# Performance work log

Hardware: AMD Instinct MI355X
Metric: run time of the kernel (lower is better)

The kernel has to match this reference:

```python
import jax, jax.numpy as jnp
import numpy as np

N = 200000   # nodes (Elliptic-scale)
E = 500000   # directed edges
F = 166      # in_channels / node feature dim
H = 128      # hidden_channels
C = 2        # out_channels
T = 49       # number of time steps


def setup_inputs() -> dict:
    key = jax.random.key(0)
    ks = jax.random.split(key, 12)
    x = jax.random.normal(ks[0], (N, F), jnp.float32)
    edge_index = jax.random.randint(ks[1], (2, E), 0, N, dtype=jnp.int32)
    time_step = jax.random.randint(ks[2], (N,), 0, T, dtype=jnp.int32)
    sF = 1.0 / np.sqrt(F)
    sH = 1.0 / np.sqrt(H)
    initial_w = jax.random.uniform(ks[3], (F, F), jnp.float32, -sF, sF)
    gru_w_ih = jax.random.uniform(ks[4], (3 * F, F), jnp.float32, -sF, sF)
    gru_w_hh = jax.random.uniform(ks[5], (3 * F, F), jnp.float32, -sF, sF)
    gru_b_ih = jax.random.uniform(ks[6], (3 * F,), jnp.float32, -sF, sF)
    gru_b_hh = jax.random.uniform(ks[7], (3 * F,), jnp.float32, -sF, sF)
    proj_w = jax.random.uniform(ks[8], (H, F), jnp.float32, -sF, sF)
    proj_b = jax.random.uniform(ks[9], (H,), jnp.float32, -sF, sF)
    cls_w = jax.random.uniform(ks[10], (C, H), jnp.float32, -sH, sH)
    cls_b = jax.random.uniform(ks[11], (C,), jnp.float32, -sH, sH)
    return {"x": x, "edge_index": edge_index, "time_step": time_step,
            "initial_w": initial_w, "gru_w_ih": gru_w_ih, "gru_w_hh": gru_w_hh,
            "gru_b_ih": gru_b_ih, "gru_b_hh": gru_b_hh,
            "proj_w": proj_w, "proj_b": proj_b, "cls_w": cls_w, "cls_b": cls_b}


def reference(x, edge_index, time_step, initial_w, gru_w_ih, gru_w_hh,
              gru_b_ih, gru_b_hh, proj_w, proj_b, cls_w, cls_b):
    src, dst = edge_index[0], edge_index[1]
    n = x.shape[0]

    def gru(W):
        # torch.nn.GRU single step, input = hidden = W  (FxF matrix, rows = batch)
        gi = W @ gru_w_ih.T + gru_b_ih
        gh = W @ gru_w_hh.T + gru_b_hh
        i_r, i_z, i_n = jnp.split(gi, 3, axis=-1)
        h_r, h_z, h_n = jnp.split(gh, 3, axis=-1)
        r = jax.nn.sigmoid(i_r + h_r)
        z = jax.nn.sigmoid(i_z + h_z)
        nn_ = jnp.tanh(i_n + r * h_n)
        return (1.0 - z) * nn_ + z * W

    def step(carry, t):
        W, logits = carry
        W = gru(W)  # evolve GCN weight (EvolveGCN-O)
        # subgraph of nodes with time_step <= t, expressed by masking (same math
        # as relabel+extract: inactive nodes contribute nothing, their outputs are ignored)
        act = time_step <= t
        ew = (act[src] & act[dst]).astype(x.dtype)
        # gcn_norm with self-loops: deg = in-degree over active edges + 1
        deg = jax.ops.segment_sum(ew, dst, num_segments=n) + 1.0
        dinv = jax.lax.rsqrt(deg)
        norm = ew * dinv[src] * dinv[dst]
        h = jnp.where(act[:, None], x, 0.0) @ W               # [N, F]
        agg = jax.ops.segment_sum(h[src] * norm[:, None], dst, num_segments=n)
        agg = agg + h / deg[:, None]                          # self-loop term dinv_i^2 * h_i
        z = jax.nn.relu(agg @ proj_w.T + proj_b)              # [N, H] (dropout: eval mode)
        lg = z @ cls_w.T + cls_b                              # [N, C]
        logits = jnp.where((time_step == t)[:, None], lg, logits)
        return (W, logits), None

    init = (initial_w, jnp.zeros((n, cls_w.shape[0]), x.dtype))
    (_, logits), _ = jax.lax.scan(step, init, jnp.arange(T, dtype=time_step.dtype))
    return logits
```

## Files before the change

kernel.cpp:

```cpp
#include <hip/hip_runtime.h>
#include <hip/hip_fp16.h>
#include <math.h>

#define NN 200000
#define NE 500000
#define FF 166
#define HH 128
#define CC 2
#define TT 49
#define GG 498
#define PADN 203136
#define MAXTILES 6400
#define KP 84
#define KPAD 192
#define SCB 512
#define SNB 391
#define HB 782
#define CIB 1954
#define XSB 37500
#define ECB 782
#define P2B 210
#define C2B 977
#define H2B 391
#define DEGB 782
#define MBB (TT * 96)

typedef _Float16 half2v __attribute__((ext_vector_type(2)));
typedef _Float16 f16x4 __attribute__((ext_vector_type(4)));
typedef _Float16 f16x8 __attribute__((ext_vector_type(8)));
typedef float f32x4 __attribute__((ext_vector_type(4)));
typedef unsigned long long u64;

static __device__ __forceinline__ float fdot2f(half2v a, half2v b, float c) {
#if __has_builtin(__builtin_amdgcn_fdot2)
    return __builtin_amdgcn_fdot2(a, b, c, false);
#else
    return c + (float)a.x * (float)b.x + (float)a.y * (float)b.y;
#endif
}

__global__ __launch_bounds__(512) void setup1(
        const float* __restrict__ wih, const float* __restrict__ whh,
        const float* __restrict__ projw,
        _Float16* __restrict__ wkp, float* __restrict__ projwT,
        const int* __restrict__ dstp, int* __restrict__ offc,
        const int* __restrict__ ts, int* __restrict__ cnt, int* __restrict__ rank) {
    __shared__ int h2[2][TT];
    int b = blockIdx.x;
    int tid = threadIdx.x;
    if (b < P2B) {
        int idx = b * 512 + tid;
        const int A = 2 * KP * 512;
        if (idx < A) {
            int m = idx / (KP * 512);
            int r = idx - m * (KP * 512);
            int kp = r >> 9, c = r & 511;
            const float* Wm = m ? whh : wih;
            float x0 = 0.0f, x1 = 0.0f;
            if (c < GG) {
                int k0 = 2 * kp, k1 = 2 * kp + 1;
                if (k0 < FF) x0 = Wm[c * FF + k0];
                if (k1 < FF) x1 = Wm[c * FF + k1];
            }
            wkp[2 * idx]     = (_Float16)x0;
            wkp[2 * idx + 1] = (_Float16)x1;
        } else if (idx < A + FF * HH) {
            int q = idx - A;
            int k = q >> 7, hh = q & 127;
            projwT[q] = projw[hh * FF + k];
        }
    } else if (b < P2B + C2B) {
        int e = (b - P2B) * 512 + tid;
        if (e < NE) atomicAdd(&offc[dstp[e]], 1);
    } else {
        int hb2 = b - P2B - C2B;
        int sub = tid >> 8;
        int lt = tid & 255;
        if (lt < TT) h2[sub][lt] = 0;
        __syncthreads();
        int i = hb2 * 512 + tid;
        if (i < NN) {
            int t = ts[i];
            rank[i] = atomicAdd(&h2[sub][t], 1);
        }
        __syncthreads();
        if (lt < TT) cnt[(hb2 * 2 + sub) * TT + lt] = h2[sub][lt];
    }
}

__global__ __launch_bounds__(512) void setup2g(
        const float* __restrict__ initial_w, const _Float16* __restrict__ wkp,
        const float* __restrict__ bih, const float* __restrict__ bhh,
        float* __restrict__ W_all,
        const int* __restrict__ off, int* __restrict__ bsum,
        const int* __restrict__ cnt, int* __restrict__ basecol, int* __restrict__ bcnt) {
    __shared__ float s_w[FF];
    __shared__ __align__(16) _Float16 s_wh[2 * KP];
    __shared__ float s_pre[2][512];
    __shared__ int s[512];
    int tid = threadIdx.x;
    int b = blockIdx.x;

    if (b < FF) {
        int row = b;
        if (tid < FF) {
            float v = initial_w[(size_t)row * FF + tid];
            s_w[tid] = v;
            s_wh[tid] = (_Float16)v;
        } else if (tid < 2 * KP) {
            s_wh[tid] = (_Float16)0.0f;
        }
        int cc0 = tid * 2;
        bool act = cc0 < 996;
        int m = (cc0 >= 498) ? 1 : 0;
        int c0 = act ? (cc0 - m * 498) : 0;
        half2v wr0[KP], wr1[KP];
        {
            const half2v* __restrict__ pW =
                (const half2v*)wkp + (size_t)(act ? m : 0) * (KP * 512) + c0;
            #pragma unroll
            for (int kp = 0; kp < KP; ++kp) {
                wr0[kp] = pW[(size_t)(kp << 9)];
                wr1[kp] = pW[(size_t)(kp << 9) + 1];
            }
        }
        float bi_r = 0, bi_z = 0, bi_n = 0, bh_r = 0, bh_z = 0, bh_n = 0;
        if (tid < FF) {
            bi_r = bih[tid]; bi_z = bih[FF + tid]; bi_n = bih[2 * FF + tid];
            bh_r = bhh[tid]; bh_z = bhh[FF + tid]; bh_n = bhh[2 * FF + tid];
        }
        __syncthreads();
        const f16x8* s_wh8 = (const f16x8*)s_wh;
        for (int t = 0; t < TT; ++t) {
            if (act) {
                float a0 = 0.0f, a1 = 0.0f;
                #pragma unroll
                for (int q = 0; q < 21; ++q) {
                    f16x8 w8 = s_wh8[q];
                    half2v h0 = __builtin_shufflevector(w8, w8, 0, 1);
                    half2v h1 = __builtin_shufflevector(w8, w8, 2, 3);
                    half2v h2v = __builtin_shufflevector(w8, w8, 4, 5);
                    half2v h3 = __builtin_shufflevector(w8, w8, 6, 7);
                    a0 = fdot2f(wr0[4 * q + 0], h0, a0);  a1 = fdot2f(wr1[4 * q + 0], h0, a1);
                    a0 = fdot2f(wr0[4 * q + 1], h1, a0);  a1 = fdot2f(wr1[4 * q + 1], h1, a1);
                    a0 = fdot2f(wr0[4 * q + 2], h2v, a0); a1 = fdot2f(wr1[4 * q + 2], h2v, a1);
                    a0 = fdot2f(wr0[4 * q + 3], h3, a0);  a1 = fdot2f(wr1[4 * q + 3], h3, a1);
                }
                s_pre[m][c0]     = a0;
                s_pre[m][c0 + 1] = a1;
            }
            __syncthreads();
            if (tid < FF) {
                float i_r = s_pre[0][tid]          + bi_r;
                float h_r = s_pre[1][tid]          + bh_r;
                float i_z = s_pre[0][FF + tid]     + bi_z;
                float h_z = s_pre[1][FF + tid]     + bh_z;
                float i_n = s_pre[0][2 * FF + tid] + bi_n;
                float h_n = s_pre[1][2 * FF + tid] + bh_n;
                float rg = 1.0f / (1.0f + expf(-(i_r + h_r)));
                float zg = 1.0f / (1.0f + expf(-(i_z + h_z)));
                float ng = tanhf(i_n + rg * h_n);
                float wnew = (1.0f - zg) * ng + zg * s_w[tid];
                s_w[tid] = wnew;
                s_wh[tid] = (_Float16)wnew;
                W_all[((size_t)t * FF + row) * FF + tid] = wnew;
            }
            __syncthreads();
        }
    } else if (b < FF + SNB) {
        int bb = b - FF;
        int i = bb * SCB + tid;
        s[tid] = (i < NN) ? off[i] : 0;
        __syncthreads();
        for (int d = 256; d > 0; d >>= 1) {
            if (tid < d) s[tid] += s[tid + d];
            __syncthreads();
        }
        if (tid == 0) bsum[bb] = s[0];
    } else {
        int t = b - FF - SNB;
        int b0 = tid * 2;
        int v0 = (b0 < HB) ? cnt[b0 * TT + t] : 0;
        int v1 = (b0 + 1 < HB) ? cnt[(b0 + 1) * TT + t] : 0;
        int sum = v0 + v1;
        s[tid] = sum;
        __syncthreads();
        for (int d = 1; d < 512; d <<= 1) {
            int u = (tid >= d) ? s[tid - d] : 0;
            __syncthreads();
            s[tid] += u;
            __syncthreads();
        }
        int base = s[tid] - sum;
        if (b0 < HB) basecol[b0 * TT + t] = base;
        if (b0 + 1 < HB) basecol[(b0 + 1) * TT + t] = base + v0;
        if (tid == 511) bcnt[t] = s[511];
    }
}

__global__ __launch_bounds__(512) void setup3(
        const int* __restrict__ bsum, int* __restrict__ bpre, int* __restrict__ off,
        const int* __restrict__ bcnt, int* __restrict__ pstart,
        int* __restrict__ tile_t, int* __restrict__ tile_r0, int* __restrict__ meta) {
    __shared__ int s[512];
    int tid = threadIdx.x;
    if (blockIdx.x == 0) {
        int v = (tid < SNB) ? bsum[tid] : 0;
        s[tid] = v;
        __syncthreads();
        for (int d = 1; d < 512; d <<= 1) {
            int u = (tid >= d) ? s[tid - d] : 0;
            __syncthreads();
            s[tid] += u;
            __syncthreads();
        }
        bpre[tid] = s[tid] - v;
        if (tid == 511) off[NN] = s[511];
    } else {
        int t = tid;
        int nt = (t < TT) ? (bcnt[t] + 31) / 32 : 0;
        if (t < 64) s[t] = nt;
        __syncthreads();
        for (int d = 1; d < 64; d <<= 1) {
            int v = (t >= d && t < 64) ? s[t - d] : 0;
            __syncthreads();
            if (t < 64) s[t] += v;
            __syncthreads();
        }
        if (t < 64) {
            int ntbase = s[t] - nt;
            int pbase = ntbase * 32;
            if (t < TT) {
                pstart[t] = pbase;
                for (int u = 0; u < nt; ++u) {
                    tile_t[ntbase + u] = t;
                    tile_r0[ntbase + u] = pbase + u * 32;
                }
            }
            if (t == 63) {
                meta[0] = s[63];
                meta[1] = s[63] * 32;
                pstart[TT] = s[63] * 32;
            }
        }
    }
}

__global__ __launch_bounds__(512) void setup4(
        int* __restrict__ off, const int* __restrict__ bpre,
        const int* __restrict__ ts, const int* __restrict__ rank,
        const int* __restrict__ basecol, const int* __restrict__ pstart,
        int* __restrict__ perm, int* __restrict__ pos) {
    __shared__ int s[512];
    int b = blockIdx.x, tid = threadIdx.x;
    if (b < SNB) {
        int i = b * SCB + tid;
        int v = (i < NN) ? off[i] : 0;
        s[tid] = v;
        __syncthreads();
        for (int d = 1; d < 512; d <<= 1) {
            int u = (tid >= d) ? s[tid - d] : 0;
            __syncthreads();
            s[tid] += u;
            __syncthreads();
        }
        if (i < NN) off[i] = s[tid] - v + bpre[b];
    } else {
        int i = (b - SNB) * 512 + tid;
        if (i < NN) {
            int t = ts[i];
            int hb = i >> 8;
            int p = pstart[t] + basecol[hb * TT + t] + rank[i];
            perm[p] = i;
            pos[i] = p;
        }
    }
}

__global__ __launch_bounds__(256) void fill_adj(
        const int* __restrict__ srcp, const int* __restrict__ dstp,
        const int* __restrict__ ts, const int* __restrict__ off,
        int* __restrict__ cursor, int2* __restrict__ adjst,
        const int* __restrict__ pos) {
    int e = blockIdx.x * 256 + threadIdx.x;
    if (e < NE) {
        int d = dstp[e];
        int s2 = srcp[e];
        int p = atomicAdd(&cursor[d], 1);
        adjst[off[d] + p] = make_int2(s2, (ts[s2] << 25) | pos[s2]);
    }
}

__global__ __launch_bounds__(256) void degf_m(
        const int* __restrict__ off, const int2* __restrict__ adjst,
        const int* __restrict__ ts, _Float16* __restrict__ dinvh,
        float* __restrict__ selfdeg,
        const float* __restrict__ W_all, const float* __restrict__ projwT,
        _Float16* __restrict__ Mh) {
    __shared__ unsigned short sh[TT * 256];
    __shared__ __align__(16) float sw2[2][168];
    int b = blockIdx.x;
    int tid = threadIdx.x;
    if (b < DEGB) {
        int i = b * 256 + tid;
        for (int t = 0; t < TT; ++t) sh[t * 256 + tid] = 0;
        if (i >= NN) return;
        int tsi = ts[i];
        int e0 = off[i], e1 = off[i + 1];
        for (int e = e0; e < e1; ++e) {
            int tj = adjst[e].y >> 25;
            sh[tj * 256 + tid]++;
        }
        int cum = 1;
        for (int t = 0; t < TT; ++t) {
            cum += sh[t * 256 + tid];
            dinvh[(size_t)t * NN + i] = (_Float16)rsqrtf((float)cum);
            if (t == tsi) selfdeg[i] = 1.0f / (float)cum;
        }
    } else {
        int mb = b - DEGB;
        int t = mb / 96, rb = mb - t * 96;
        int r0 = rb * 2;
        for (int idx = tid; idx < 2 * FF; idx += 256) {
            int rr = idx / FF, k = idx - rr * FF;
            int r = r0 + rr;
            sw2[rr][k] = (r < FF) ? W_all[((size_t)t * FF + r) * FF + k] : 0.0f;
        }
        __syncthreads();
        int rr = tid >> 7, h = tid & 127;
        int r = r0 + rr;
        float acc = 0.0f;
        if (r < FF) {
            const float* __restrict__ pw = projwT + h;
            #pragma unroll 4
            for (int c4 = 0; c4 < 164; c4 += 4) {
                float4 w = *(const float4*)&sw2[rr][c4];
                acc += w.x * pw[(size_t)(c4 + 0) << 7];
                acc += w.y * pw[(size_t)(c4 + 1) << 7];
                acc += w.z * pw[(size_t)(c4 + 2) << 7];
                acc += w.w * pw[(size_t)(c4 + 3) << 7];
            }
            acc += sw2[rr][164] * pw[(size_t)164 << 7];
            acc += sw2[rr][165] * pw[(size_t)165 << 7];
        }
        Mh[((size_t)t * HH + h) * KPAD + r] = (_Float16)acc;
    }
}

__global__ __launch_bounds__(256) void setup6(
        const int* __restrict__ off, const int2* __restrict__ adjst,
        const int* __restrict__ ts, const _Float16* __restrict__ dinvh,
        int2* __restrict__ ewp, int* __restrict__ nact,
        const float* __restrict__ x, const int* __restrict__ pos,
        f16x4* __restrict__ x2p4) {
    int b = blockIdx.x, tid = threadIdx.x;
    if (b < ECB) {
        int i = b * 256 + tid;
        if (i >= NN) return;
        int t = ts[i];
        const _Float16* dv = dinvh + (size_t)t * NN;
        float dvi = (float)dv[i];
        int e0 = off[i], e1 = off[i + 1];
        int c = e0;
        for (int e = e0; e < e1; ++e) {
            int2 a = adjst[e];
            if ((a.y >> 25) <= t) {
                float w = (float)dv[a.x] * dvi;
                ewp[c++] = make_int2(a.y & 0x1FFFFFF, __float_as_int(w));
            }
        }
        nact[i] = c - e0;
    } else {
        int idx = (b - ECB) * 256 + tid;
        if (idx >= NN * 48) return;
        int i = idx / 48, cp4 = idx - i * 48;
        int c0 = cp4 * 4;
        const float* xr = x + (size_t)i * FF;
        union { u64 u; float f[2]; } p0, p1;
        p0.u = 0; p1.u = 0;
        if (c0 + 3 < FF) {
            p0.u = __builtin_nontemporal_load((const u64*)(xr + c0));
            p1.u = __builtin_nontemporal_load((const u64*)(xr + c0 + 2));
        } else if (c0 < FF) {
            p0.u = __builtin_nontemporal_load((const u64*)(xr + c0));
        }
        f16x4 h;
        h[0] = (_Float16)p0.f[0]; h[1] = (_Float16)p0.f[1];
        h[2] = (_Float16)p1.f[0]; h[3] = (_Float16)p1.f[1];
        x2p4[(size_t)pos[i] * 48 + cp4] = h;
    }
}

__global__ __launch_bounds__(512) void gemm_fused5(
        const int* __restrict__ meta, const int* __restrict__ tile_t,
        const int* __restrict__ tile_r0, const int* __restrict__ perm,
        const float* __restrict__ selfdeg, const f16x4* __restrict__ x2p4,
        const int* __restrict__ off, const int* __restrict__ nact,
        const int2* __restrict__ ewp,
        const _Float16* __restrict__ Mh, const float* __restrict__ proj_b,
        const float* __restrict__ cls_w, const float* __restrict__ cls_b,
        float* __restrict__ out) {
    __shared__ __align__(16) char smraw[32 * 130 * 4];
    _Float16* sY = (_Float16*)smraw;
    float* sP = (float*)smraw;
    int bid = blockIdx.x;
    if (bid >= meta[0]) return;
    int t = tile_t[bid], r0 = tile_r0[bid];
    int tid = threadIdx.x;
    int lane = tid & 63;
    int w = tid >> 6;
    bool ln48 = lane < 48;

    {
        const uint4* src = (const uint4*)(x2p4 + (size_t)r0 * 48);
        #pragma unroll
        for (int u = 0; u < 2; ++u) {
            int q = tid + u * 512;
            if (q < 768) {
                int row = q / 24, kc = q - row * 24;
                *(uint4*)(sY + row * 200 + kc * 8) = src[q];
            }
        }
    }
    __syncthreads();

    int rbase = w * 4;
    int ep[4], ee[4];
    float ac[4][4];
    #pragma unroll
    for (int q = 0; q < 4; ++q) {
        int r = rbase + q;
        int i = perm[r0 + r];
        float sw = 0.0f;
        ep[q] = 0; ee[q] = 0;
        if (i >= 0) {
            sw = selfdeg[i];
            ep[q] = off[i];
            ee[q] = ep[q] + nact[i];
        }
        f16x4 h = (f16x4)((_Float16)0.0f);
        if (ln48) h = *(const f16x4*)(sY + r * 200 + lane * 4);
        ac[q][0] = sw * (float)h[0];
        ac[q][1] = sw * (float)h[1];
        ac[q][2] = sw * (float)h[2];
        ac[q][3] = sw * (float)h[3];
    }
    int2 pc[4];
    #pragma unroll
    for (int q = 0; q < 4; ++q) pc[q] = (ep[q] < ee[q]) ? ewp[ep[q]] : make_int2(0, 0);
    while ((ep[0] < ee[0]) | (ep[1] < ee[1]) | (ep[2] < ee[2]) | (ep[3] < ee[3])) {
        int js[4]; float wv[4];
        #pragma unroll
        for (int q = 0; q < 4; ++q) {
            bool val = ep[q] < ee[q];
            js[q] = pc[q].x;
            wv[q] = val ? __int_as_float(pc[q].y) : 0.0f;
            if (val) ep[q]++;
        }
        #pragma unroll
        for (int q = 0; q < 4; ++q) pc[q] = (ep[q] < ee[q]) ? ewp[ep[q]] : make_int2(0, 0);
        #pragma unroll
        for (int q = 0; q < 4; ++q) {
            if (wv[q] != 0.0f && ln48) {
                f16x4 g = x2p4[(size_t)js[q] * 48 + lane];
                ac[q][0] += wv[q] * (float)g[0];
                ac[q][1] += wv[q] * (float)g[1];
                ac[q][2] += wv[q] * (float)g[2];
                ac[q][3] += wv[q] * (float)g[3];
            }
        }
    }
    #pragma unroll
    for (int q = 0; q < 4; ++q) {
        if (ln48) {
            f16x4 o;
            o[0] = (_Float16)ac[q][0];
            o[1] = (_Float16)ac[q][1];
            o[2] = (_Float16)ac[q][2];
            o[3] = (_Float16)ac[q][3];
            *(f16x4*)(sY + (rbase + q) * 200 + lane * 4) = o;
        }
    }
    __syncthreads();

    int lr = lane & 15;
    int kg = lane >> 4;
    int c0 = w * 16;
    f32x4 acc0 = {0, 0, 0, 0}, acc1 = {0, 0, 0, 0};
    const _Float16* B0 = Mh + ((size_t)t * HH + c0 + lr) * KPAD + kg * 8;
    const _Float16* A0 = sY + lr * 200 + kg * 8;
    const _Float16* A1 = A0 + 16 * 200;

    #pragma unroll
    for (int s = 0; s < 6; ++s) {
        f16x8 b0 = *(const f16x8*)(B0 + s * 32);
        f16x8 a0 = *(const f16x8*)(A0 + s * 32);
        f16x8 a1 = *(const f16x8*)(A1 + s * 32);
        acc0 = __builtin_amdgcn_mfma_f32_16x16x32_f16(a0, b0, acc0, 0, 0, 0);
        acc1 = __builtin_amdgcn_mfma_f32_16x16x32_f16(a1, b0, acc1, 0, 0, 0);
    }

    float pb = proj_b[c0 + lr];
    __syncthreads();
    int prow = kg * 4;
    int colw = c0 + lr;
    #pragma unroll
    for (int r = 0; r < 4; ++r) {
        sP[(prow + r) * 130 + colw]      = fmaxf(acc0[r] + pb, 0.0f);
        sP[(16 + prow + r) * 130 + colw] = fmaxf(acc1[r] + pb, 0.0f);
    }
    __syncthreads();

    int row = tid >> 4, cc = (tid >> 3) & 1, qq = tid & 7;
    const float* pr = sP + row * 130 + qq * 16;
    const float* cw = cls_w + cc * HH + qq * 16;
    float s = 0.0f;
    #pragma unroll
    for (int h = 0; h < 16; ++h) s += pr[h] * cw[h];
    s += __shfl_xor(s, 1);
    s += __shfl_xor(s, 2);
    s += __shfl_xor(s, 4);
    if (qq == 0) {
        int node = perm[r0 + row];
        if (node >= 0) out[(size_t)node * CC + cc] = s + cls_b[cc];
    }
}

extern "C" void kernel_launch(void* const* d_in, const int* in_sizes, int n_in,
                              void* d_out, int out_size, void* d_ws, size_t ws_size,
                              hipStream_t stream) {
    const float* x = (const float*)d_in[0];
    const int* ei = (const int*)d_in[1];
    const int* srcp = ei;
    const int* dstp = ei + NE;
    const int* ts = (const int*)d_in[2];
    const float* initial_w = (const float*)d_in[3];
    const float* wih = (const float*)d_in[4];
    const float* whh = (const float*)d_in[5];
    const float* bih = (const float*)d_in[6];
    const float* bhh = (const float*)d_in[7];
    const float* projw = (const float*)d_in[8];
    const float* projb = (const float*)d_in[9];
    const float* clsw = (const float*)d_in[10];
    const float* clsb = (const float*)d_in[11];
    float* out = (float*)d_out;

    char* base = (char*)d_ws;
    size_t o = 0;
    auto alloc = [&](size_t bytes) { size_t r = o; o = (o + bytes + 255) & ~(size_t)255; return r; };

    float*    W_all   = (float*)   (base + alloc((size_t)TT * FF * FF * 4));
    _Float16* Mh      = (_Float16*)(base + alloc((size_t)TT * HH * KPAD * 2));
    _Float16* wkp     = (_Float16*)(base + alloc((size_t)2 * KP * 512 * 2 * 2));
    float*    projwT  = (float*)   (base + alloc((size_t)FF * HH * 4));
    int*      off     = (int*)     (base + alloc((size_t)(NN + 1) * 4));
    int*      cursor  = (int*)     (base + alloc((size_t)NN * 4));
    int2*     adjst   = (int2*)    (base + alloc((size_t)NE * 8));
    int2*     ewp     = (int2*)    (base + alloc((size_t)NE * 8));
    _Float16* dinvh   = (_Float16*)(base + alloc((size_t)TT * NN * 2));
    float*    selfdeg = (float*)   (base + alloc((size_t)NN * 4));
    int*      nact    = (int*)     (base + alloc((size_t)NN * 4));
    int*      pos     = (int*)     (base + alloc((size_t)NN * 4));
    int*      bcnt    = (int*)     (base + alloc((size_t)TT * 4));
    int*      pstart  = (int*)     (base + alloc((size_t)(TT + 1) * 4));
    int*      meta    = (int*)     (base + alloc(2 * 4));
    int*      tile_t  = (int*)     (base + alloc((size_t)MAXTILES * 4));
    int*      tile_r0 = (int*)     (base + alloc((size_t)MAXTILES * 4));
    int*      perm    = (int*)     (base + alloc((size_t)PADN * 4));
    int*      bsum    = (int*)     (base + alloc((size_t)512 * 4));
    int*      bpre    = (int*)     (base + alloc((size_t)520 * 4));
    int*      cnt     = (int*)     (base + alloc((size_t)HB * TT * 4));
    int*      basecol = (int*)     (base + alloc((size_t)HB * TT * 4));
    int*      rank    = (int*)     (base + alloc((size_t)NN * 4));
    f16x4*    x2p4    = (f16x4*)   (base + alloc((size_t)PADN * 48 * 8));

    hipMemsetAsync(off, 0, (size_t)((char*)cursor - (char*)off) + (size_t)NN * 4, stream);
    hipMemsetAsync(perm, 0xFF, (size_t)PADN * 4, stream);

    setup1<<<P2B + C2B + H2B, 512, 0, stream>>>(wih, whh, projw, wkp, projwT,
                                                dstp, off, ts, cnt, rank);
    setup2g<<<FF + SNB + TT, 512, 0, stream>>>(initial_w, wkp, bih, bhh, W_all,
                                               off, bsum, cnt, basecol, bcnt);
    setup3<<<2, 512, 0, stream>>>(bsum, bpre, off, bcnt, pstart, tile_t, tile_r0, meta);
    setup4<<<SNB + SNB, 512, 0, stream>>>(off, bpre, ts, rank, basecol, pstart, perm, pos);
    fill_adj<<<CIB, 256, 0, stream>>>(srcp, dstp, ts, off, cursor, adjst, pos);
    degf_m<<<DEGB + MBB, 256, 0, stream>>>(off, adjst, ts, dinvh, selfdeg, W_all, projwT, Mh);
    setup6<<<ECB + XSB, 256, 0, stream>>>(off, adjst, ts, dinvh, ewp, nact, x, pos, x2p4);

    gemm_fused5<<<MAXTILES, 512, 0, stream>>>(meta, tile_t, tile_r0, perm, selfdeg,
                                              x2p4, off, nact, ewp, Mh, projb, clsw, clsb, out);
}
```

Before: 318.4 us.

## Build per-time degree counts directly and pack only active edges without CSR

Replaces the full CSR adjacency build (fill_adj, then per-node scans in degf_m and setup6) with atomics into a dense [T,N] degree-count array and an active-degree count per destination. Edge weights are then written straight into an active-only CSR. The Mh projection work moves into setup3 with 4 rows per block, so the pipeline drops two kernel launches and the intermediate adjst array. In exchange it memsets and scans a 39 MB degcnt buffer, and more global atomics run in setup1.

```diff
diff --git a/kernel.cpp b/kernel.cpp
--- a/kernel.cpp
+++ b/kernel.cpp
@@ -18,12 +18,10 @@
 #define HB 782
 #define CIB 1954
 #define XSB 37500
-#define ECB 782
 #define P2B 210
 #define C2B 977
 #define H2B 391
-#define DEGB 782
-#define MBB (TT * 96)
+#define MB3 (TT * 48)
 
 typedef _Float16 half2v __attribute__((ext_vector_type(2)));
 typedef _Float16 f16x4 __attribute__((ext_vector_type(4)));
@@ -43,8 +41,10 @@
         const float* __restrict__ wih, const float* __restrict__ whh,
         const float* __restrict__ projw,
         _Float16* __restrict__ wkp, float* __restrict__ projwT,
-        const int* __restrict__ dstp, int* __restrict__ offc,
-        const int* __restrict__ ts, int* __restrict__ cnt, int* __restrict__ rank) {
+        const int* __restrict__ srcp, const int* __restrict__ dstp,
+        const int* __restrict__ ts,
+        int* __restrict__ degcnt, int* __restrict__ actdeg,
+        int* __restrict__ cnt, int* __restrict__ rank) {
     __shared__ int h2[2][TT];
     int b = blockIdx.x;
     int tid = threadIdx.x;
@@ -71,7 +71,13 @@
         }
     } else if (b < P2B + C2B) {
         int e = (b - P2B) * 512 + tid;
-        if (e < NE) atomicAdd(&offc[dstp[e]], 1);
+        if (e < NE) {
+            int d = dstp[e];
+            int s2 = srcp[e];
+            int tsrc = ts[s2];
+            atomicAdd(&degcnt[(size_t)tsrc * NN + d], 1);
+            if (tsrc <= ts[d]) atomicAdd(&actdeg[d], 1);
+        }
     } else {
         int hb2 = b - P2B - C2B;
         int sub = tid >> 8;
@@ -92,8 +98,10 @@
         const float* __restrict__ initial_w, const _Float16* __restrict__ wkp,
         const float* __restrict__ bih, const float* __restrict__ bhh,
         float* __restrict__ W_all,
-        const int* __restrict__ off, int* __restrict__ bsum,
-        const int* __restrict__ cnt, int* __restrict__ basecol, int* __restrict__ bcnt) {
+        const int* __restrict__ actdeg, int* __restrict__ bsum,
+        const int* __restrict__ cnt, int* __restrict__ basecol, int* __restrict__ bcnt,
+        const int* __restrict__ degcnt, const int* __restrict__ ts,
+        _Float16* __restrict__ dinvh, float* __restrict__ selfdeg) {
     __shared__ float s_w[FF];
     __shared__ __align__(16) _Float16 s_wh[2 * KP];
     __shared__ float s_pre[2][512];
@@ -170,14 +178,14 @@
     } else if (b < FF + SNB) {
         int bb = b - FF;
         int i = bb * SCB + tid;
-        s[tid] = (i < NN) ? off[i] : 0;
+        s[tid] = (i < NN) ? actdeg[i] : 0;
         __syncthreads();
         for (int d = 256; d > 0; d >>= 1) {
             if (tid < d) s[tid] += s[tid + d];
             __syncthreads();
         }
         if (tid == 0) bsum[bb] = s[0];
-    } else {
+    } else if (b < FF + SNB + TT) {
         int t = b - FF - SNB;
         int b0 = tid * 2;
         int v0 = (b0 < HB) ? cnt[b0 * TT + t] : 0;
@@ -195,16 +203,31 @@
         if (b0 < HB) basecol[b0 * TT + t] = base;
         if (b0 + 1 < HB) basecol[(b0 + 1) * TT + t] = base + v0;
         if (tid == 511) bcnt[t] = s[511];
+    } else {
+        int i = (b - FF - SNB - TT) * 512 + tid;
+        if (i < NN) {
+            int tsi = ts[i];
+            int cum = 1;
+            for (int t = 0; t < TT; ++t) {
+                cum += degcnt[(size_t)t * NN + i];
+                dinvh[(size_t)t * NN + i] = (_Float16)rsqrtf((float)cum);
+                if (t == tsi) selfdeg[i] = 1.0f / (float)cum;
+            }
+        }
     }
 }
 
 __global__ __launch_bounds__(512) void setup3(
-        const int* __restrict__ bsum, int* __restrict__ bpre, int* __restrict__ off,
+        const int* __restrict__ bsum, int* __restrict__ bpre,
         const int* __restrict__ bcnt, int* __restrict__ pstart,
-        int* __restrict__ tile_t, int* __restrict__ tile_r0, int* __restrict__ meta) {
+        int* __restrict__ tile_t, int* __restrict__ tile_r0, int* __restrict__ meta,
+        const float* __restrict__ W_all, const float* __restrict__ projwT,
+        _Float16* __restrict__ Mh) {
     __shared__ int s[512];
+    __shared__ __align__(16) float sw4[4][168];
     int tid = threadIdx.x;
-    if (blockIdx.x == 0) {
+    int b = blockIdx.x;
+    if (b == 0) {
         int v = (tid < SNB) ? bsum[tid] : 0;
         s[tid] = v;
         __syncthreads();
@@ -215,8 +238,7 @@
             __syncthreads();
         }
         bpre[tid] = s[tid] - v;
-        if (tid == 511) off[NN] = s[511];
-    } else {
+    } else if (b == 1) {
         int t = tid;
         int nt = (t < TT) ? (bcnt[t] + 31) / 32 : 0;
         if (t < 64) s[t] = nt;
@@ -243,11 +265,39 @@
                 pstart[TT] = s[63] * 32;
             }
         }
+    } else {
+        int mb = b - 2;
+        int t = mb / 48, rb = mb - t * 48;
+        int r0 = rb * 4;
+        for (int idx = tid; idx < 4 * FF; idx += 512) {
+            int rr = idx / FF, k = idx - rr * FF;
+            int r = r0 + rr;
+            sw4[rr][k] = (r < FF) ? W_all[((size_t)t * FF + r) * FF + k] : 0.0f;
+        }
+        __syncthreads();
+        int rr = tid >> 7, h = tid & 127;
+        int r = r0 + rr;
+        float acc = 0.0f;
+        if (r < FF) {
+            const float* __restrict__ pw = projwT + h;
+            #pragma unroll 4
+            for (int c4 = 0; c4 < 164; c4 += 4) {
+                float4 w = *(const float4*)&sw4[rr][c4];
+                acc += w.x * pw[(size_t)(c4 + 0) << 7];
+                acc += w.y * pw[(size_t)(c4 + 1) << 7];
+                acc += w.z * pw[(size_t)(c4 + 2) << 7];
+                acc += w.w * pw[(size_t)(c4 + 3) << 7];
+            }
+            acc += sw4[rr][164] * pw[(size_t)164 << 7];
+            acc += sw4[rr][165] * pw[(size_t)165 << 7];
+        }
+        Mh[((size_t)t * HH + h) * KPAD + r] = (_Float16)acc;
     }
 }
 
 __global__ __launch_bounds__(512) void setup4(
-        int* __restrict__ off, const int* __restrict__ bpre,
+        const int* __restrict__ actdeg, const int* __restrict__ bpre,
+        int* __restrict__ aoff,
         const int* __restrict__ ts, const int* __restrict__ rank,
         const int* __restrict__ basecol, const int* __restrict__ pstart,
         int* __restrict__ perm, int* __restrict__ pos) {
@@ -255,7 +305,7 @@
     int b = blockIdx.x, tid = threadIdx.x;
     if (b < SNB) {
         int i = b * SCB + tid;
-        int v = (i < NN) ? off[i] : 0;
+        int v = (i < NN) ? actdeg[i] : 0;
         s[tid] = v;
         __syncthreads();
         for (int d = 1; d < 512; d <<= 1) {
@@ -264,7 +314,7 @@
             s[tid] += u;
             __syncthreads();
         }
-        if (i < NN) off[i] = s[tid] - v + bpre[b];
+        if (i < NN) aoff[i] = s[tid] - v + bpre[b];
     } else {
         int i = (b - SNB) * 512 + tid;
         if (i < NN) {
@@ -277,101 +327,28 @@
     }
 }
 
-__global__ __launch_bounds__(256) void fill_adj(
+__global__ __launch_bounds__(256) void setup5(
         const int* __restrict__ srcp, const int* __restrict__ dstp,
-        const int* __restrict__ ts, const int* __restrict__ off,
-        int* __restrict__ cursor, int2* __restrict__ adjst,
-        const int* __restrict__ pos) {
-    int e = blockIdx.x * 256 + threadIdx.x;
-    if (e < NE) {
-        int d = dstp[e];
-        int s2 = srcp[e];
-        int p = atomicAdd(&cursor[d], 1);
-        adjst[off[d] + p] = make_int2(s2, (ts[s2] << 25) | pos[s2]);
-    }
-}
-
-__global__ __launch_bounds__(256) void degf_m(
-        const int* __restrict__ off, const int2* __restrict__ adjst,
-        const int* __restrict__ ts, _Float16* __restrict__ dinvh,
-        float* __restrict__ selfdeg,
-        const float* __restrict__ W_all, const float* __restrict__ projwT,
-        _Float16* __restrict__ Mh) {
-    __shared__ unsigned short sh[TT * 256];
-    __shared__ __align__(16) float sw2[2][168];
-    int b = blockIdx.x;
-    int tid = threadIdx.x;
-    if (b < DEGB) {
-        int i = b * 256 + tid;
-        for (int t = 0; t < TT; ++t) sh[t * 256 + tid] = 0;
-        if (i >= NN) return;
-        int tsi = ts[i];
-        int e0 = off[i], e1 = off[i + 1];
-        for (int e = e0; e < e1; ++e) {
-            int tj = adjst[e].y >> 25;
-            sh[tj * 256 + tid]++;
-        }
-        int cum = 1;
-        for (int t = 0; t < TT; ++t) {
-            cum += sh[t * 256 + tid];
-            dinvh[(size_t)t * NN + i] = (_Float16)rsqrtf((float)cum);
-            if (t == tsi) selfdeg[i] = 1.0f / (float)cum;
+        const int* __restrict__ ts, const _Float16* __restrict__ dinvh,
+        const int* __restrict__ aoff, int* __restrict__ cursor,
+        const int* __restrict__ pos, int2* __restrict__ ewp,
+        const float* __restrict__ x, f16x4* __restrict__ x2p4) {
+    int b = blockIdx.x, tid = threadIdx.x;
+    if (b < CIB) {
+        int e = b * 256 + tid;
+        if (e < NE) {
+            int d = dstp[e];
+            int s2 = srcp[e];
+            int t = ts[d];
+            if (ts[s2] <= t) {
+                const _Float16* dv = dinvh + (size_t)t * NN;
+                float w = (float)dv[s2] * (float)dv[d];
+                int p = atomicAdd(&cursor[d], 1);
+                ewp[aoff[d] + p] = make_int2(pos[s2], __float_as_int(w));
+            }
         }
     } else {
-        int mb = b - DEGB;
-        int t = mb / 96, rb = mb - t * 96;
-        int r0 = rb * 2;
-        for (int idx = tid; idx < 2 * FF; idx += 256) {
-            int rr = idx / FF, k = idx - rr * FF;
-            int r = r0 + rr;
-            sw2[rr][k] = (r < FF) ? W_all[((size_t)t * FF + r) * FF + k] : 0.0f;
-        }
-        __syncthreads();
-        int rr = tid >> 7, h = tid & 127;
-        int r = r0 + rr;
-        float acc = 0.0f;
-        if (r < FF) {
-            const float* __restrict__ pw = projwT + h;
-            #pragma unroll 4
-            for (int c4 = 0; c4 < 164; c4 += 4) {
-                float4 w = *(const float4*)&sw2[rr][c4];
-                acc += w.x * pw[(size_t)(c4 + 0) << 7];
-                acc += w.y * pw[(size_t)(c4 + 1) << 7];
-                acc += w.z * pw[(size_t)(c4 + 2) << 7];
-                acc += w.w * pw[(size_t)(c4 + 3) << 7];
-            }
-            acc += sw2[rr][164] * pw[(size_t)164 << 7];
-            acc += sw2[rr][165] * pw[(size_t)165 << 7];
-        }
-        Mh[((size_t)t * HH + h) * KPAD + r] = (_Float16)acc;
-    }
-}
-
-__global__ __launch_bounds__(256) void setup6(
-        const int* __restrict__ off, const int2* __restrict__ adjst,
-        const int* __restrict__ ts, const _Float16* __restrict__ dinvh,
-        int2* __restrict__ ewp, int* __restrict__ nact,
-        const float* __restrict__ x, const int* __restrict__ pos,
-        f16x4* __restrict__ x2p4) {
-    int b = blockIdx.x, tid = threadIdx.x;
-    if (b < ECB) {
-        int i = b * 256 + tid;
-        if (i >= NN) return;
-        int t = ts[i];
-        const _Float16* dv = dinvh + (size_t)t * NN;
-        float dvi = (float)dv[i];
-        int e0 = off[i], e1 = off[i + 1];
-        int c = e0;
-        for (int e = e0; e < e1; ++e) {
-            int2 a = adjst[e];
-            if ((a.y >> 25) <= t) {
-                float w = (float)dv[a.x] * dvi;
-                ewp[c++] = make_int2(a.y & 0x1FFFFFF, __float_as_int(w));
-            }
-        }
-        nact[i] = c - e0;
-    } else {
-        int idx = (b - ECB) * 256 + tid;
+        int idx = (b - CIB) * 256 + tid;
         if (idx >= NN * 48) return;
         int i = idx / 48, cp4 = idx - i * 48;
         int c0 = cp4 * 4;
@@ -395,7 +372,7 @@
         const int* __restrict__ meta, const int* __restrict__ tile_t,
         const int* __restrict__ tile_r0, const int* __restrict__ perm,
         const float* __restrict__ selfdeg, const f16x4* __restrict__ x2p4,
-        const int* __restrict__ off, const int* __restrict__ nact,
+        const int* __restrict__ aoff, const int* __restrict__ actdeg,
         const int2* __restrict__ ewp,
         const _Float16* __restrict__ Mh, const float* __restrict__ proj_b,
         const float* __restrict__ cls_w, const float* __restrict__ cls_b,
@@ -435,8 +412,8 @@
         ep[q] = 0; ee[q] = 0;
         if (i >= 0) {
             sw = selfdeg[i];
-            ep[q] = off[i];
-            ee[q] = ep[q] + nact[i];
+            ep[q] = aoff[i];
+            ee[q] = ep[q] + actdeg[i];
         }
         f16x4 h = (f16x4)((_Float16)0.0f);
         if (ln48) h = *(const f16x4*)(sY + r * 200 + lane * 4);
@@ -553,13 +530,13 @@
     _Float16* Mh      = (_Float16*)(base + alloc((size_t)TT * HH * KPAD * 2));
     _Float16* wkp     = (_Float16*)(base + alloc((size_t)2 * KP * 512 * 2 * 2));
     float*    projwT  = (float*)   (base + alloc((size_t)FF * HH * 4));
-    int*      off     = (int*)     (base + alloc((size_t)(NN + 1) * 4));
     int*      cursor  = (int*)     (base + alloc((size_t)NN * 4));
-    int2*     adjst   = (int2*)    (base + alloc((size_t)NE * 8));
+    int*      actdeg  = (int*)     (base + alloc((size_t)NN * 4));
+    int*      degcnt  = (int*)     (base + alloc((size_t)TT * NN * 4));
     int2*     ewp     = (int2*)    (base + alloc((size_t)NE * 8));
     _Float16* dinvh   = (_Float16*)(base + alloc((size_t)TT * NN * 2));
     float*    selfdeg = (float*)   (base + alloc((size_t)NN * 4));
-    int*      nact    = (int*)     (base + alloc((size_t)NN * 4));
+    int*      aoff    = (int*)     (base + alloc((size_t)NN * 4));
     int*      pos     = (int*)     (base + alloc((size_t)NN * 4));
     int*      bcnt    = (int*)     (base + alloc((size_t)TT * 4));
     int*      pstart  = (int*)     (base + alloc((size_t)(TT + 1) * 4));
@@ -574,19 +551,21 @@
     int*      rank    = (int*)     (base + alloc((size_t)NN * 4));
     f16x4*    x2p4    = (f16x4*)   (base + alloc((size_t)PADN * 48 * 8));
 
-    hipMemsetAsync(off, 0, (size_t)((char*)cursor - (char*)off) + (size_t)NN * 4, stream);
+    hipMemsetAsync(cursor, 0, (size_t)((char*)degcnt - (char*)cursor) + (size_t)TT * NN * 4, stream);
     hipMemsetAsync(perm, 0xFF, (size_t)PADN * 4, stream);
 
     setup1<<<P2B + C2B + H2B, 512, 0, stream>>>(wih, whh, projw, wkp, projwT,
-                                                dstp, off, ts, cnt, rank);
-    setup2g<<<FF + SNB + TT, 512, 0, stream>>>(initial_w, wkp, bih, bhh, W_all,
-                                               off, bsum, cnt, basecol, bcnt);
-    setup3<<<2, 512, 0, stream>>>(bsum, bpre, off, bcnt, pstart, tile_t, tile_r0, meta);
-    setup4<<<SNB + SNB, 512, 0, stream>>>(off, bpre, ts, rank, basecol, pstart, perm, pos);
-    fill_adj<<<CIB, 256, 0, stream>>>(srcp, dstp, ts, off, cursor, adjst, pos);
-    degf_m<<<DEGB + MBB, 256, 0, stream>>>(off, adjst, ts, dinvh, selfdeg, W_all, projwT, Mh);
-    setup6<<<ECB + XSB, 256, 0, stream>>>(off, adjst, ts, dinvh, ewp, nact, x, pos, x2p4);
+                                                srcp, dstp, ts, degcnt, actdeg, cnt, rank);
+    setup2g<<<FF + SNB + TT + SNB, 512, 0, stream>>>(initial_w, wkp, bih, bhh, W_all,
+                                                     actdeg, bsum, cnt, basecol, bcnt,
+                                                     degcnt, ts, dinvh, selfdeg);
+    setup3<<<2 + MB3, 512, 0, stream>>>(bsum, bpre, bcnt, pstart, tile_t, tile_r0, meta,
+                                        W_all, projwT, Mh);
+    setup4<<<SNB + SNB, 512, 0, stream>>>(actdeg, bpre, aoff, ts, rank, basecol,
+                                          pstart, perm, pos);
+    setup5<<<CIB + XSB, 256, 0, stream>>>(srcp, dstp, ts, dinvh, aoff, cursor, pos, ewp,
+                                          x, x2p4);
 
     gemm_fused5<<<MAXTILES, 512, 0, stream>>>(meta, tile_t, tile_r0, perm, selfdeg,
-                                              x2p4, off, nact, ewp, Mh, projb, clsw, clsb, out);
-}
+                                              x2p4, aoff, actdeg, ewp, Mh, projb, clsw, clsb, out);
+}
```

Measured after the change: 338.2 us. 6.2% more time.
